# Kernel optimization log

Hardware: AMD Instinct MI355X
Metric: run time of the kernel (lower is better)

Reference implementation:

```python
import jax, jax.numpy as jnp
import numpy as np

N = 100000      # num_nodes
E = 1600000     # num_edges (avg degree 16)
D_IN = 128
D_H = 128
D_OUT = 128


def _init_linear(key, out_dim, in_dim):
    # Kaiming-uniform-like init, bound = 1/sqrt(fan_in)
    bound = 1.0 / np.sqrt(in_dim)
    return jax.random.uniform(key, (out_dim, in_dim), jnp.float32, -bound, bound)


def setup_inputs() -> dict:
    key = jax.random.key(0)
    ks = jax.random.split(key, 12)
    x = jax.random.normal(ks[0], (N, D_IN), jnp.float32)
    edge_index = jax.random.randint(ks[1], (2, E), 0, N, jnp.int32)
    dims = [(D_H, D_IN), (D_H, D_H), (D_OUT, D_H)]
    inp = {"x": x, "edge_index": edge_index}
    for i, (do, di) in enumerate(dims):
        inp[f"Wl{i}"] = _init_linear(ks[2 + 3 * i], do, di)      # lin_l: applied to aggregated neighbors
        inp[f"bl{i}"] = jnp.zeros((do,), jnp.float32)
        inp[f"Wr{i}"] = _init_linear(ks[3 + 3 * i], do, di)      # lin_r: applied to root (self) features
    return inp


def _sage_conv(x, src, dst, Wl, bl, Wr):
    # mean aggregation of source-node features at destination nodes
    msg = x[src]                                                   # [E, d]
    agg = jax.ops.segment_sum(msg, dst, num_segments=N)            # [N, d]
    deg = jax.ops.segment_sum(jnp.ones((src.shape[0],), x.dtype), dst, num_segments=N)
    mean = agg / jnp.maximum(deg, 1.0)[:, None]
    return mean @ Wl.T + bl + x @ Wr.T


def reference(x, edge_index, Wl0, bl0, Wr0, Wl1, bl1, Wr1, Wl2, bl2, Wr2):
    src, dst = edge_index[0], edge_index[1]
    # dropout is identity in eval mode
    h = jax.nn.relu(_sage_conv(x, src, dst, Wl0, bl0, Wr0))
    h = jax.nn.relu(_sage_conv(h, src, dst, Wl1, bl1, Wr1))
    return _sage_conv(h, src, dst, Wl2, bl2, Wr2)
```

## Files before the change

### kernel.cpp

```cpp
#include <hip/hip_runtime.h>
#include <hip/hip_bf16.h>

typedef __attribute__((ext_vector_type(8))) short bf16x8;
typedef __attribute__((ext_vector_type(4))) float f32x4;
typedef __attribute__((ext_vector_type(2))) float f32x2;

#define D 128
#define BCAP 8192


__global__ __launch_bounds__(256) void k_mega(
    const float* __restrict__ x,
    const float* __restrict__ w0, const float* __restrict__ w1,
    const float* __restrict__ w2, const float* __restrict__ w3,
    const float* __restrict__ w4, const float* __restrict__ w5,
    __hip_bfloat16* __restrict__ xb, __hip_bfloat16* __restrict__ wb,
    int* __restrict__ bcursor, int* __restrict__ tmp,
    const int* __restrict__ src, const int* __restrict__ dst,
    int xpair, int e, int n, int p1b, int epb)
{
    if (blockIdx.x < p1b) {
        __shared__ int lh[512], gb[512];
        for (int i = threadIdx.x; i < 512; i += 256) lh[i] = 0;
        __syncthreads();
        int lo = blockIdx.x * epb;
        int hi = lo + epb; if (hi > e) hi = e;
        for (int i = lo + threadIdx.x; i < hi; i += 256) {
            int d = dst[i]; d = ((unsigned)d < (unsigned)n) ? d : 0;
            atomicAdd(&lh[d >> 8], 1);
        }
        __syncthreads();
        for (int i = threadIdx.x; i < 512; i += 256) {
            int c = lh[i];
            gb[i] = c ? atomicAdd(&bcursor[i], c) : 0;
        }
        __syncthreads();
        for (int i = threadIdx.x; i < 512; i += 256) lh[i] = 0;
        __syncthreads();
        for (int i = lo + threadIdx.x; i < hi; i += 256) {
            int d = dst[i]; d = ((unsigned)d < (unsigned)n) ? d : 0;
            int s = src[i]; s = ((unsigned)s < (unsigned)n) ? s : 0;
            int b = d >> 8;
            int p = gb[b] + atomicAdd(&lh[b], 1);
            if (p < BCAP)
                tmp[b * BCAP + p] = s | ((d & 255) << 17);
        }
    } else {
        int t = (blockIdx.x - p1b) * 256 + threadIdx.x;
        if (t < xpair) {
            float2 f = ((const float2*)x)[t];
            ((__hip_bfloat162*)xb)[t] = __float22bfloat162_rn(f);
        }
        if (t < 6 * 8192) {
            int wsel = t >> 13, wi = t & 8191;
            const float* wp = w0;
            if (wsel == 1) wp = w1;
            else if (wsel == 2) wp = w2;
            else if (wsel == 3) wp = w3;
            else if (wsel == 4) wp = w4;
            else if (wsel == 5) wp = w5;
            float2 f = ((const float2*)wp)[wi];
            ((__hip_bfloat162*)wb)[t] = __float22bfloat162_rn(f);
        }
    }
}


__global__ __launch_bounds__(256) void k_p2(const int* __restrict__ tmp,
                                            const int* __restrict__ bcnt,
                                            int* __restrict__ deg, int* __restrict__ offs,
                                            int* __restrict__ csr, int n) {
    __shared__ int hist[256], loc[256], cur[256];
    __shared__ int out[BCAP];
    int b = blockIdx.x, t = threadIdx.x;
    int base = b * BCAP;
    int cnt = bcnt[b]; if (cnt > BCAP) cnt = BCAP;
    int nodes = n - b * 256; if (nodes > 256) nodes = 256;
    hist[t] = 0;
    __syncthreads();
    for (int i = t; i < cnt; i += 256)
        atomicAdd(&hist[(tmp[base + i] >> 17) & 255], 1);
    __syncthreads();
    int v = hist[t];
    loc[t] = v;
    __syncthreads();
    for (int off = 1; off < 256; off <<= 1) {
        int x = (t >= off) ? loc[t - off] : 0;
        __syncthreads();
        loc[t] += x;
        __syncthreads();
    }
    int myloc = loc[t] - v;
    cur[t] = myloc;
    if (t < nodes) { deg[b * 256 + t] = v; offs[b * 256 + t] = base + myloc; }
    __syncthreads();
    for (int i = t; i < cnt; i += 256) {
        int e = tmp[base + i];
        int p = atomicAdd(&cur[(e >> 17) & 255], 1);
        out[p] = e & 0x1FFFF;
    }
    __syncthreads();
    for (int i = t; i < cnt; i += 256) csr[base + i] = out[i];
}


__device__ __forceinline__ void acc_u32(f32x2& a, unsigned p) {
    f32x2 c;
    c.x = __uint_as_float(p << 16);
    c.y = __uint_as_float(p & 0xffff0000u);
    a += c;
}

__device__ __forceinline__ void acc_i4(f32x2* acc, int4 d) {
    acc_u32(acc[0], (unsigned)d.x);
    acc_u32(acc[1], (unsigned)d.y);
    acc_u32(acc[2], (unsigned)d.z);
    acc_u32(acc[3], (unsigned)d.w);
}

__global__ __launch_bounds__(256) void k_agg(
    const __hip_bfloat16* __restrict__ h,
    const int* __restrict__ csr,
    const int* __restrict__ offs,
    const int* __restrict__ deg,
    __hip_bfloat16* __restrict__ mean,
    int n)
{
    int node = blockIdx.x * 4 + (threadIdx.x >> 6);
    int lane = threadIdx.x & 63;
    if (node >= n) return;
    int grp = lane >> 4;
    int sub = lane & 15;
    int start = offs[node];
    int cnt = deg[node];

    f32x2 acc[4];
    #pragma unroll
    for (int k = 0; k < 4; ++k) acc[k] = (f32x2){0.f, 0.f};

    const char* hb = (const char*)h;
    unsigned suboff = (unsigned)sub * 16u;
    const int* cp = csr + start + grp;

    int i = 0;
    int bulk = cnt & ~15;

    for (; i < bulk; i += 16) {
        int s[4];
        #pragma unroll
        for (int u = 0; u < 4; ++u) s[u] = cp[i + u * 4];
        int4 d[4];
        #pragma unroll
        for (int u = 0; u < 4; ++u)
            d[u] = *(const int4*)(hb + (((unsigned)s[u] << 8) | suboff));
        #pragma unroll
        for (int u = 0; u < 4; ++u) acc_i4(acc, d[u]);
    }

    if (i < cnt) {
        int4 d[4];
        #pragma unroll
        for (int u = 0; u < 4; ++u) {
            int e = i + u * 4 + grp;
            int ec = (e < cnt) ? e : (cnt - 1);
            int s = csr[start + ec];
            d[u] = *(const int4*)(hb + (((unsigned)s << 8) | suboff));
            if (e >= cnt) d[u] = make_int4(0, 0, 0, 0);
        }
        #pragma unroll
        for (int u = 0; u < 4; ++u) acc_i4(acc, d[u]);
    }

    #pragma unroll
    for (int k = 0; k < 4; ++k) {
        acc[k].x += __shfl_xor(acc[k].x, 16);
        acc[k].y += __shfl_xor(acc[k].y, 16);
        acc[k].x += __shfl_xor(acc[k].x, 32);
        acc[k].y += __shfl_xor(acc[k].y, 32);
    }

    if (grp == 0) {
        float inv = 1.0f / fmaxf((float)cnt, 1.0f);
        union { int4 i4; __hip_bfloat162 h2[4]; } u;
        #pragma unroll
        for (int k = 0; k < 4; ++k)
            u.h2[k] = __float22bfloat162_rn(make_float2(acc[k].x * inv, acc[k].y * inv));
        *(int4*)((char*)mean + (size_t)node * 256 + suboff) = u.i4;
    }
}


__global__ __launch_bounds__(512) void k_gemm(
    const __hip_bfloat16* __restrict__ A0,
    const __hip_bfloat16* __restrict__ A1,
    const __hip_bfloat16* __restrict__ Wb,
    const float* __restrict__ bias,
    float* __restrict__ outF,
    __hip_bfloat16* __restrict__ outB,
    int n, int do_relu)
{
    __shared__ __hip_bfloat16 lW[2 * 128 * 128];

    for (int g = threadIdx.x; g < 4096; g += 512) {
        int half = g >> 11;
        int rem  = g & 2047;
        int row  = rem >> 4;
        int c    = rem & 15;
        bf16x8 v = *(const bf16x8*)(Wb + half * 16384 + row * 128 + c * 8);
        *(bf16x8*)(lW + half * 16384 + row * 128 + ((c ^ (row & 7)) * 8)) = v;
    }
    __syncthreads();

    int w = threadIdx.x >> 6;
    int lane = threadIdx.x & 63;
    int m = lane & 15;
    int q = lane >> 4;
    int base = blockIdx.x * 256 + w * 32;

    f32x4 acc[2][8];
    #pragma unroll
    for (int r = 0; r < 2; ++r)
        #pragma unroll
        for (int i = 0; i < 8; ++i) acc[r][i] = (f32x4){0.f, 0.f, 0.f, 0.f};

    const __hip_bfloat16* Aps[2] = {A0, A1};

    #pragma unroll
    for (int half = 0; half < 2; ++half) {
        const __hip_bfloat16* A = Aps[half];
        #pragma unroll
        for (int kk = 0; kk < 4; ++kk) {
            bf16x8 af[2];
            #pragma unroll
            for (int r = 0; r < 2; ++r) {
                int arow = base + r * 16 + m;
                if (arow > n - 1) arow = n - 1;
                af[r] = *(const bf16x8*)(A + (size_t)arow * D + kk * 32 + q * 8);
            }
            #pragma unroll
            for (int nt = 0; nt < 8; ++nt) {
                int row = nt * 16 + m;
                int c = (kk * 4 + q) ^ (m & 7);
                bf16x8 bf = *(const bf16x8*)(lW + half * 16384 + row * 128 + c * 8);
                #pragma unroll
                for (int r = 0; r < 2; ++r)
                    acc[r][nt] = __builtin_amdgcn_mfma_f32_16x16x32_bf16(af[r], bf, acc[r][nt], 0, 0, 0);
            }
        }
    }

    #pragma unroll
    for (int r = 0; r < 2; ++r) {
        #pragma unroll
        for (int nt = 0; nt < 8; ++nt) {
            int col = nt * 16 + m;
            float b = bias[col];
            #pragma unroll
            for (int rr = 0; rr < 4; ++rr) {
                int row = base + r * 16 + q * 4 + rr;
                if (row < n) {
                    float v = acc[r][nt][rr] + b;
                    if (do_relu) v = fmaxf(v, 0.f);
                    if (outF) outF[(size_t)row * D + col] = v;
                    else      outB[(size_t)row * D + col] = __float2bfloat16(v);
                }
            }
        }
    }
}


extern "C" void kernel_launch(void* const* d_in, const int* in_sizes, int n_in,
                              void* d_out, int out_size, void* d_ws, size_t ws_size,
                              hipStream_t stream) {
    const float* x   = (const float*)d_in[0];
    const int*   ei  = (const int*)d_in[1];
    const float* Wl0 = (const float*)d_in[2];
    const float* bl0 = (const float*)d_in[3];
    const float* Wr0 = (const float*)d_in[4];
    const float* Wl1 = (const float*)d_in[5];
    const float* bl1 = (const float*)d_in[6];
    const float* Wr1 = (const float*)d_in[7];
    const float* Wl2 = (const float*)d_in[8];
    const float* bl2 = (const float*)d_in[9];
    const float* Wr2 = (const float*)d_in[10];

    const int n = in_sizes[0] / D;
    const int e = in_sizes[1] / 2;
    const int* src = ei;
    const int* dst = ei + e;
    const int nb = (n + 255) >> 8;

    uintptr_t p = ((uintptr_t)d_ws + 255) & ~(uintptr_t)255;
    auto carve = [&](size_t bytes) {
        uintptr_t r = p;
        p = (p + bytes + 255) & ~(uintptr_t)255;
        return (void*)r;
    };
    int* deg     = (int*)carve((size_t)n * 4);
    int* offs    = (int*)carve((size_t)n * 4);
    int* bcursor = (int*)carve(512 * 4);
    __hip_bfloat16* mean = (__hip_bfloat16*)carve((size_t)n * D * 2);
    __hip_bfloat16* F1   = (__hip_bfloat16*)carve((size_t)n * D * 2);
    __hip_bfloat16* Wb   = (__hip_bfloat16*)carve((size_t)6 * D * D * 2);
    (void)ws_size; (void)n_in; (void)out_size;

    __hip_bfloat16* h0 = (__hip_bfloat16*)d_out;
    int* tmp = (int*)((char*)d_out + (size_t)n * D * 2);

    const int xpair = n * D / 2;

    hipMemsetAsync(bcursor, 0, 512 * 4, stream);
    const int p1b = 782;
    const int epb = 2048;
    const int megag = p1b + (xpair + 255) / 256;
    k_mega<<<megag, 256, 0, stream>>>(
        x, Wl0, Wr0, Wl1, Wr1, Wl2, Wr2, F1, Wb, bcursor, tmp, src, dst,
        xpair, e, n, p1b, epb);

    k_p2<<<nb, 256, 0, stream>>>(tmp, bcursor, deg, offs, tmp, n);

    const int ag = (n + 3) / 4;
    const int gg = (n + 255) / 256;

    __hip_bfloat16* Wb0 = Wb + 0 * 2 * D * D;
    __hip_bfloat16* Wb1 = Wb + 1 * 2 * D * D;
    __hip_bfloat16* Wb2 = Wb + 2 * 2 * D * D;

    k_agg<<<ag, 256, 0, stream>>>(F1, tmp, offs, deg, mean, n);
    k_gemm<<<gg, 512, 0, stream>>>(mean, F1, Wb0, bl0, nullptr, h0, n, 1);
    k_agg<<<ag, 256, 0, stream>>>(h0, tmp, offs, deg, mean, n);
    k_gemm<<<gg, 512, 0, stream>>>(mean, h0, Wb1, bl1, nullptr, F1, n, 1);
    k_agg<<<ag, 256, 0, stream>>>(F1, tmp, offs, deg, mean, n);
    k_gemm<<<gg, 512, 0, stream>>>(mean, F1, Wb2, bl2, (float*)d_out, nullptr, n, 0);
}
```

Baseline: 395.7 us.

## Replace global-atomic bucket scatter with per-block sorted runs and run-info gather

Edge bucketing in the first pass drops the global bcursor atomics and scattered writes. Each block now sorts its edge chunk by bucket in shared memory, writes it out contiguously, and records a per-bucket offset and count in a runinfo table. The second pass prefix-scans these runs and gathers each bucket's edges into shared memory before building the CSR, which also removes the memset. The x and weight conversion to bf16 is widened to float4 loads. The trade-off is a serial per-thread gather loop in k_p2 that may be unbalanced, plus an extra runinfo buffer placed in the output scratch space.

```diff
diff --git a/kernel.cpp b/kernel.cpp
--- a/kernel.cpp
+++ b/kernel.cpp
@@ -7,6 +7,8 @@
 
 #define D 128
 #define BCAP 8192
+#define EPB 3125
+#define SBMAX 512
 
 
 __global__ __launch_bounds__(256) void k_mega(
@@ -15,71 +17,123 @@
     const float* __restrict__ w2, const float* __restrict__ w3,
     const float* __restrict__ w4, const float* __restrict__ w5,
     __hip_bfloat16* __restrict__ xb, __hip_bfloat16* __restrict__ wb,
-    int* __restrict__ bcursor, int* __restrict__ tmp,
+    int* __restrict__ gbuf, int* __restrict__ runinfo,
     const int* __restrict__ src, const int* __restrict__ dst,
-    int xpair, int e, int n, int p1b, int epb)
+    int xquad, int e, int n, int p1b)
 {
     if (blockIdx.x < p1b) {
-        __shared__ int lh[512], gb[512];
-        for (int i = threadIdx.x; i < 512; i += 256) lh[i] = 0;
-        __syncthreads();
-        int lo = blockIdx.x * epb;
-        int hi = lo + epb; if (hi > e) hi = e;
-        for (int i = lo + threadIdx.x; i < hi; i += 256) {
+        __shared__ int lh[512], lpre[512], pscan[256];
+        __shared__ int lout[3328];
+        int t = threadIdx.x;
+        lh[t] = 0; lh[t + 256] = 0;
+        __syncthreads();
+        int lo = blockIdx.x * EPB;
+        int hi = lo + EPB; if (hi > e) hi = e;
+        for (int i = lo + t; i < hi; i += 256) {
             int d = dst[i]; d = ((unsigned)d < (unsigned)n) ? d : 0;
             atomicAdd(&lh[d >> 8], 1);
         }
         __syncthreads();
-        for (int i = threadIdx.x; i < 512; i += 256) {
-            int c = lh[i];
-            gb[i] = c ? atomicAdd(&bcursor[i], c) : 0;
-        }
-        __syncthreads();
-        for (int i = threadIdx.x; i < 512; i += 256) lh[i] = 0;
-        __syncthreads();
-        for (int i = lo + threadIdx.x; i < hi; i += 256) {
+        int c0 = lh[2 * t], c1 = lh[2 * t + 1];
+        int pair = c0 + c1;
+        pscan[t] = pair;
+        __syncthreads();
+        for (int off = 1; off < 256; off <<= 1) {
+            int v = (t >= off) ? pscan[t - off] : 0;
+            __syncthreads();
+            pscan[t] += v;
+            __syncthreads();
+        }
+        int excl = pscan[t] - pair;
+        lpre[2 * t] = excl;
+        lpre[2 * t + 1] = excl + c0;
+        runinfo[(2 * t) * SBMAX + blockIdx.x]     = (excl << 16) | c0;
+        runinfo[(2 * t + 1) * SBMAX + blockIdx.x] = ((excl + c0) << 16) | c1;
+        lh[2 * t] = 0; lh[2 * t + 1] = 0;
+        __syncthreads();
+        for (int i = lo + t; i < hi; i += 256) {
             int d = dst[i]; d = ((unsigned)d < (unsigned)n) ? d : 0;
             int s = src[i]; s = ((unsigned)s < (unsigned)n) ? s : 0;
             int b = d >> 8;
-            int p = gb[b] + atomicAdd(&lh[b], 1);
-            if (p < BCAP)
-                tmp[b * BCAP + p] = s | ((d & 255) << 17);
-        }
+            int p = lpre[b] + atomicAdd(&lh[b], 1);
+            lout[p] = s | ((d & 255) << 17);
+        }
+        __syncthreads();
+        int cnt = hi - lo;
+        for (int i = t; i < cnt; i += 256) gbuf[lo + i] = lout[i];
     } else {
         int t = (blockIdx.x - p1b) * 256 + threadIdx.x;
-        if (t < xpair) {
-            float2 f = ((const float2*)x)[t];
-            ((__hip_bfloat162*)xb)[t] = __float22bfloat162_rn(f);
-        }
-        if (t < 6 * 8192) {
-            int wsel = t >> 13, wi = t & 8191;
+        if (t < xquad) {
+            float4 f = ((const float4*)x)[t];
+            union { int2 i2; __hip_bfloat162 h2[2]; } u;
+            u.h2[0] = __float22bfloat162_rn(make_float2(f.x, f.y));
+            u.h2[1] = __float22bfloat162_rn(make_float2(f.z, f.w));
+            ((int2*)xb)[t] = u.i2;
+        }
+        if (t < 6 * 4096) {
+            int wsel = t >> 12, wi = t & 4095;
             const float* wp = w0;
             if (wsel == 1) wp = w1;
             else if (wsel == 2) wp = w2;
             else if (wsel == 3) wp = w3;
             else if (wsel == 4) wp = w4;
             else if (wsel == 5) wp = w5;
-            float2 f = ((const float2*)wp)[wi];
-            ((__hip_bfloat162*)wb)[t] = __float22bfloat162_rn(f);
-        }
-    }
-}
-
-
-__global__ __launch_bounds__(256) void k_p2(const int* __restrict__ tmp,
-                                            const int* __restrict__ bcnt,
-                                            int* __restrict__ deg, int* __restrict__ offs,
-                                            int* __restrict__ csr, int n) {
+            float4 f = ((const float4*)wp)[wi];
+            union { int2 i2; __hip_bfloat162 h2[2]; } u;
+            u.h2[0] = __float22bfloat162_rn(make_float2(f.x, f.y));
+            u.h2[1] = __float22bfloat162_rn(make_float2(f.z, f.w));
+            ((int2*)wb)[t] = u.i2;
+        }
+    }
+}
+
+
+__global__ __launch_bounds__(256) void k_p2(
+    const int* __restrict__ gbuf, const int* __restrict__ runinfo,
+    int* __restrict__ deg, int* __restrict__ offs,
+    int* __restrict__ csr, int n, int p1b)
+{
+    __shared__ int ebuf[BCAP];
+    __shared__ int out[BCAP];
+    __shared__ int pscan[256];
     __shared__ int hist[256], loc[256], cur[256];
-    __shared__ int out[BCAP];
     int b = blockIdx.x, t = threadIdx.x;
-    int base = b * BCAP;
-    int cnt = bcnt[b]; if (cnt > BCAP) cnt = BCAP;
+
+    int sb0 = 2 * t, sb1 = 2 * t + 1;
+    int r0 = (sb0 < p1b) ? runinfo[b * SBMAX + sb0] : 0;
+    int r1 = (sb1 < p1b) ? runinfo[b * SBMAX + sb1] : 0;
+    int l0 = r0 & 0xffff, l1 = r1 & 0xffff;
+    int pair = l0 + l1;
+    pscan[t] = pair;
+    __syncthreads();
+    for (int off = 1; off < 256; off <<= 1) {
+        int v = (t >= off) ? pscan[t - off] : 0;
+        __syncthreads();
+        pscan[t] += v;
+        __syncthreads();
+    }
+    int excl = pscan[t] - pair;
+    int cnt = pscan[255];
+    if (cnt > BCAP) cnt = BCAP;
+
+    if (excl < BCAP) {
+        int s0 = sb0 * EPB + (r0 >> 16);
+        int lim0 = (excl + l0 <= BCAP) ? l0 : (BCAP - excl);
+        for (int k = 0; k < lim0; ++k) ebuf[excl + k] = gbuf[s0 + k];
+        int o1 = excl + l0;
+        if (o1 < BCAP) {
+            int s1 = sb1 * EPB + (r1 >> 16);
+            int lim1 = (o1 + l1 <= BCAP) ? l1 : (BCAP - o1);
+            for (int k = 0; k < lim1; ++k) ebuf[o1 + k] = gbuf[s1 + k];
+        }
+    }
+    __syncthreads();
+
     int nodes = n - b * 256; if (nodes > 256) nodes = 256;
     hist[t] = 0;
     __syncthreads();
     for (int i = t; i < cnt; i += 256)
-        atomicAdd(&hist[(tmp[base + i] >> 17) & 255], 1);
+        atomicAdd(&hist[(ebuf[i] >> 17) & 255], 1);
     __syncthreads();
     int v = hist[t];
     loc[t] = v;
@@ -92,15 +146,15 @@
     }
     int myloc = loc[t] - v;
     cur[t] = myloc;
-    if (t < nodes) { deg[b * 256 + t] = v; offs[b * 256 + t] = base + myloc; }
+    if (t < nodes) { deg[b * 256 + t] = v; offs[b * 256 + t] = b * BCAP + myloc; }
     __syncthreads();
     for (int i = t; i < cnt; i += 256) {
-        int e = tmp[base + i];
-        int p = atomicAdd(&cur[(e >> 17) & 255], 1);
-        out[p] = e & 0x1FFFF;
-    }
-    __syncthreads();
-    for (int i = t; i < cnt; i += 256) csr[base + i] = out[i];
+        int ed = ebuf[i];
+        int p = atomicAdd(&cur[(ed >> 17) & 255], 1);
+        out[p] = ed & 0x1FFFF;
+    }
+    __syncthreads();
+    for (int i = t; i < cnt; i += 256) csr[b * BCAP + i] = out[i];
 }
 
 
@@ -299,26 +353,26 @@
     };
     int* deg     = (int*)carve((size_t)n * 4);
     int* offs    = (int*)carve((size_t)n * 4);
-    int* bcursor = (int*)carve(512 * 4);
     __hip_bfloat16* mean = (__hip_bfloat16*)carve((size_t)n * D * 2);
     __hip_bfloat16* F1   = (__hip_bfloat16*)carve((size_t)n * D * 2);
     __hip_bfloat16* Wb   = (__hip_bfloat16*)carve((size_t)6 * D * D * 2);
     (void)ws_size; (void)n_in; (void)out_size;
 
-    __hip_bfloat16* h0 = (__hip_bfloat16*)d_out;
-    int* tmp = (int*)((char*)d_out + (size_t)n * D * 2);
-
-    const int xpair = n * D / 2;
-
-    hipMemsetAsync(bcursor, 0, 512 * 4, stream);
-    const int p1b = 782;
-    const int epb = 2048;
-    const int megag = p1b + (xpair + 255) / 256;
+    char* ob = (char*)d_out;
+    __hip_bfloat16* h0 = (__hip_bfloat16*)ob;
+    int* gbuf    = (int*)(ob + (size_t)n * D * 2);
+    int* runinfo = (int*)(ob + (size_t)n * D * 2 + (size_t)e * 4);
+    int* csrS    = (int*)(ob + (size_t)n * D * 2 + (size_t)e * 4 + (size_t)SBMAX * 512 * 4);
+
+    const int xquad = n * D / 4;
+    const int p1b = (e + EPB - 1) / EPB;
+
+    const int megag = p1b + (xquad + 255) / 256;
     k_mega<<<megag, 256, 0, stream>>>(
-        x, Wl0, Wr0, Wl1, Wr1, Wl2, Wr2, F1, Wb, bcursor, tmp, src, dst,
-        xpair, e, n, p1b, epb);
-
-    k_p2<<<nb, 256, 0, stream>>>(tmp, bcursor, deg, offs, tmp, n);
+        x, Wl0, Wr0, Wl1, Wr1, Wl2, Wr2, F1, Wb, gbuf, runinfo, src, dst,
+        xquad, e, n, p1b);
+
+    k_p2<<<nb, 256, 0, stream>>>(gbuf, runinfo, deg, offs, csrS, n, p1b);
 
     const int ag = (n + 3) / 4;
     const int gg = (n + 255) / 256;
@@ -327,10 +381,10 @@
     __hip_bfloat16* Wb1 = Wb + 1 * 2 * D * D;
     __hip_bfloat16* Wb2 = Wb + 2 * 2 * D * D;
 
-    k_agg<<<ag, 256, 0, stream>>>(F1, tmp, offs, deg, mean, n);
+    k_agg<<<ag, 256, 0, stream>>>(F1, csrS, offs, deg, mean, n);
     k_gemm<<<gg, 512, 0, stream>>>(mean, F1, Wb0, bl0, nullptr, h0, n, 1);
-    k_agg<<<ag, 256, 0, stream>>>(h0, tmp, offs, deg, mean, n);
+    k_agg<<<ag, 256, 0, stream>>>(h0, csrS, offs, deg, mean, n);
     k_gemm<<<gg, 512, 0, stream>>>(mean, h0, Wb1, bl1, nullptr, F1, n, 1);
-    k_agg<<<ag, 256, 0, stream>>>(F1, tmp, offs, deg, mean, n);
+    k_agg<<<ag, 256, 0, stream>>>(F1, csrS, offs, deg, mean, n);
     k_gemm<<<gg, 512, 0, stream>>>(mean, F1, Wb2, bl2, (float*)d_out, nullptr, n, 0);
 }
```

New measurement: 373.2 us. -5.7%, faster.
